# Performance work log

Hardware: AMD Instinct MI355X
Metric: run time of the kernel (lower is better)

Reference implementation:

```python
import jax, jax.numpy as jnp
import numpy as np

D_OUT = 10
N_BINS = 50
DELTA_SCALE = 60.0
TEMPERATURE = 1.0
CAND_BATCH = 1000  # hard-coded in the torch forward loop
EPS = 1e-8


def setup_inputs() -> dict:
    key = jax.random.key(0)
    ks = jax.random.split(key, 7)
    n_q, n_c, d_num, d_cat = 512, 8000, 6, 20
    return {
        "x_num": jax.random.normal(ks[0], (n_q, d_num), dtype=jnp.float32),
        "x_cat": jax.random.uniform(ks[1], (n_q, d_cat), dtype=jnp.float32),
        "candidate_x_num": jax.random.normal(ks[2], (n_c, d_num), dtype=jnp.float32),
        "candidate_x_cat": jax.random.uniform(ks[3], (n_c, d_cat), dtype=jnp.float32),
        "candidate_y": jax.random.randint(ks[4], (n_c,), 0, D_OUT, dtype=jnp.int64),
        # delta = rand(d_in_num, n_bins) * delta_scale (Parameter init)
        "delta": jax.random.uniform(ks[5], (d_num, N_BINS), dtype=jnp.float32) * DELTA_SCALE,
        # u = rand(d_in_num, n_bins) (buffer)
        "u": jax.random.uniform(ks[6], (d_num, N_BINS), dtype=jnp.float32),
    }


def _feature_map(x, delta, u):
    # x: [N, d_num] -> bin indices [N, d_num * n_bins]
    scaled_u = u * delta  # [d_num, n_bins]
    bins = jnp.ceil((x[:, :, None] - scaled_u[None]) / delta[None])
    return bins.reshape(x.shape[0], -1)


def reference(x_num, x_cat, candidate_x_num, candidate_x_cat, candidate_y, delta, u):
    x_enc = jnp.concatenate([_feature_map(x_num, delta, u), x_cat], axis=1)          # [Nq, D]
    c_enc = jnp.concatenate([_feature_map(candidate_x_num, delta, u), candidate_x_cat], axis=1)  # [Nc, D]
    y_oh = jax.nn.one_hot(candidate_y, D_OUT, dtype=jnp.float32)                     # [Nc, d_out]

    n_c, d = c_enc.shape
    n_chunks = n_c // CAND_BATCH
    c_chunks = c_enc.reshape(n_chunks, CAND_BATCH, d)
    y_chunks = y_oh.reshape(n_chunks, CAND_BATCH, D_OUT)

    def step(carry, batch):
        logits, lse = carry
        cx, cy = batch
        # L1 cdist: [Nq, CAND_BATCH]
        dist = jnp.sum(jnp.abs(x_enc[:, None, :] - cx[None, :, :]), axis=-1) / TEMPERATURE
        logits = logits + jnp.exp(-dist) @ cy
        # NOTE: faithful to torch code — per-batch logsumexp values are SUMMED
        lse = lse + jax.nn.logsumexp(-dist, axis=1)
        return (logits, lse), None

    n_q = x_enc.shape[0]
    init = (jnp.zeros((n_q, D_OUT), jnp.float32), jnp.zeros((n_q,), jnp.float32))
    (logits, lse), _ = jax.lax.scan(step, init, (c_chunks, y_chunks))
    return jnp.log(logits + EPS) - lse[:, None]
```

## Files before the change

kernel.cpp:

```cpp
#include <hip/hip_runtime.h>
#include <math.h>

#define NQ 512
#define NC 8000
#define DNUM 6
#define NBINS 50
#define DCAT 20
#define DENC 26
#define DOUT 10
#define CHUNK 1000
#define NCHUNK 8
#define QT 8
#define PSTRIDE 12

__global__ void encode(const float* __restrict__ c_num, const float* __restrict__ c_cat,
                       const float* __restrict__ x_num, const float* __restrict__ x_cat,
                       const float* __restrict__ delta, const float* __restrict__ u,
                       float* __restrict__ cEnc, float* __restrict__ qEnc) {
    int i = blockIdx.x * 256 + threadIdx.x;
    const int nA = (NC + NQ) * DNUM;
    const int nB = (NC + NQ) * DCAT;
    if (i < nA) {
        int f = i % DNUM, p = i / DNUM;
        bool is_c = p < NC;
        int idx = is_c ? p : p - NC;
        float v = (is_c ? c_num : x_num)[idx * DNUM + f];
        float g = 0.f;
        for (int j = 0; j < NBINS; ++j) {
            float dl = delta[f * NBINS + j];
            float sc = u[f * NBINS + j] * dl;
            g += ceilf((v - sc) / dl);
        }
        if (is_c) cEnc[f * NC + idx] = g;
        else      qEnc[f * NQ + idx] = g;
    } else if (i < nA + nB) {
        int i2 = i - nA;
        int k = i2 % DCAT, p = i2 / DCAT;
        bool is_c = p < NC;
        int idx = is_c ? p : p - NC;
        float v = (is_c ? c_cat : x_cat)[idx * DCAT + k];
        if (is_c) cEnc[(DNUM + k) * NC + idx] = v;
        else      qEnc[(DNUM + k) * NQ + idx] = v;
    }
}

__global__ __launch_bounds__(256) void dist_k(
    const float* __restrict__ cEnc, const float* __restrict__ qEnc,
    float* __restrict__ D) {
    __shared__ float xs[DENC * QT];
    const int tid = threadIdx.x;
    const int c = blockIdx.x * 256 + tid;
    const int q0 = blockIdx.y * QT;

    if (tid < DENC * QT) {
        int d = tid >> 3, q = tid & 7;
        xs[tid] = qEnc[d * NQ + q0 + q];
    }
    __syncthreads();

    const int cc = (c < NC) ? c : NC - 1;
    float cv[DENC];
#pragma unroll
    for (int d = 0; d < DENC; ++d) cv[d] = cEnc[(size_t)d * NC + cc];

    float acc[QT];
#pragma unroll
    for (int q = 0; q < QT; ++q) acc[q] = 0.f;
#pragma unroll
    for (int d = 0; d < DENC; ++d) {
        float cvd = cv[d];
        const float* xv = xs + d * QT;
#pragma unroll
        for (int q = 0; q < QT; ++q) acc[q] += fabsf(cvd - xv[q]);
    }
    if (c < NC) {
#pragma unroll
        for (int q = 0; q < QT; ++q) D[(size_t)(q0 + q) * NC + c] = acc[q];
    }
}

__global__ __launch_bounds__(256) void reduce_k(
    const float* __restrict__ D, const int* __restrict__ cy,
    float* __restrict__ parts) {
    __shared__ float wr[4][12];
    __shared__ float m_sh;

    const int tid = threadIdx.x;
    const int chunk = blockIdx.x;
    const int q = blockIdx.y;
    const int lane = tid & 63, wave = tid >> 6;

    const bool act = (tid < CHUNK / 4);
    const int base = chunk * CHUNK + (act ? 4 * tid : CHUNK - 4);
    float4 dv = *(const float4*)(D + (size_t)q * NC + base);
    int4 yv = *(const int4*)(cy + base);

    float v = act ? fminf(fminf(dv.x, dv.y), fminf(dv.z, dv.w)) : INFINITY;
#pragma unroll
    for (int m = 32; m >= 1; m >>= 1) v = fminf(v, __shfl_xor(v, m));
    if (lane == 0) wr[wave][0] = v;
    __syncthreads();
    if (tid == 0)
        m_sh = fminf(fminf(wr[0][0], wr[1][0]), fminf(wr[2][0], wr[3][0]));
    __syncthreads();
    const float m = m_sh;

    float r[11];
#pragma unroll
    for (int k = 0; k < 11; ++k) r[k] = 0.f;
    if (act) {
        float e0 = __expf(-dv.x), e1 = __expf(-dv.y),
              e2 = __expf(-dv.z), e3 = __expf(-dv.w);
#pragma unroll
        for (int k = 0; k < DOUT; ++k) {
            r[k] = (yv.x == k ? e0 : 0.f) + (yv.y == k ? e1 : 0.f) +
                   (yv.z == k ? e2 : 0.f) + (yv.w == k ? e3 : 0.f);
        }
        r[10] = __expf(m - dv.x) + __expf(m - dv.y) +
                __expf(m - dv.z) + __expf(m - dv.w);
    }
#pragma unroll
    for (int k = 0; k < 11; ++k) {
        float s = r[k];
#pragma unroll
        for (int mm = 32; mm >= 1; mm >>= 1) s += __shfl_xor(s, mm);
        if (lane == 0) wr[wave][k] = s;
    }
    __syncthreads();
    if (tid < 11) {
        float s = wr[0][tid] + wr[1][tid] + wr[2][tid] + wr[3][tid];
        parts[((size_t)q * NCHUNK + chunk) * PSTRIDE + tid] = s;
    }
    if (tid == 11)
        parts[((size_t)q * NCHUNK + chunk) * PSTRIDE + 11] = m;
}

__global__ void finalize(const float* __restrict__ parts, float* __restrict__ out) {
    int q = blockIdx.x * 256 + threadIdx.x;
    if (q >= NQ) return;
    float logits[DOUT];
#pragma unroll
    for (int k = 0; k < DOUT; ++k) logits[k] = 0.f;
    float lse = 0.f;
#pragma unroll
    for (int ch = 0; ch < NCHUNK; ++ch) {
        const float* p = parts + ((size_t)q * NCHUNK + ch) * PSTRIDE;
#pragma unroll
        for (int k = 0; k < DOUT; ++k) logits[k] += p[k];
        lse += logf(p[10]) - p[11];
    }
#pragma unroll
    for (int k = 0; k < DOUT; ++k)
        out[q * DOUT + k] = logf(logits[k] + 1e-8f) - lse;
}

extern "C" void kernel_launch(void* const* d_in, const int* in_sizes, int n_in,
                              void* d_out, int out_size, void* d_ws, size_t ws_size,
                              hipStream_t stream) {
    const float* x_num = (const float*)d_in[0];
    const float* x_cat = (const float*)d_in[1];
    const float* c_num = (const float*)d_in[2];
    const float* c_cat = (const float*)d_in[3];
    const int*   c_y   = (const int*)d_in[4];
    const float* delta = (const float*)d_in[5];
    const float* u     = (const float*)d_in[6];

    float* ws = (float*)d_ws;
    float* cEnc = ws;
    float* qEnc = cEnc + (size_t)DENC * NC;
    float* Dmat = qEnc + (size_t)DENC * NQ;
    float* parts = Dmat + (size_t)NQ * NC;

    const int total = (NC + NQ) * DENC;
    encode<<<(total + 255) / 256, 256, 0, stream>>>(
        c_num, c_cat, x_num, x_cat, delta, u, cEnc, qEnc);
    dist_k<<<dim3((NC + 255) / 256, NQ / QT), 256, 0, stream>>>(cEnc, qEnc, Dmat);
    reduce_k<<<dim3(NCHUNK, NQ), 256, 0, stream>>>(Dmat, c_y, parts);
    finalize<<<(NQ + 255) / 256, 256, 0, stream>>>(parts, (float*)d_out);
}
```

Before: 104.9 us.

## Fuse distance, chunk reduction and finalize into one per-query-pair kernel

Replaces the three-kernel pipeline (distance matrix written to global memory, per-chunk reduction, finalize) with a single kernel where each block handles two queries across all chunks. Distances are computed in registers and immediately reduced, so the 16 MB distance matrix round-trip and two launches go away. The in-chunk max is now combined from per-wave minima with rescaling. The trade-off is that each block rereads the whole candidate encoding with only two queries of reuse, and the launch has fewer, larger blocks.

New measurement: 105.9 us. About the same (+1.0%).

```diff
diff --git a/kernel.cpp b/kernel.cpp
--- a/kernel.cpp
+++ b/kernel.cpp
@@ -10,8 +10,6 @@
 #define DOUT 10
 #define CHUNK 1000
 #define NCHUNK 8
-#define QT 8
-#define PSTRIDE 12
 
 __global__ void encode(const float* __restrict__ c_num, const float* __restrict__ c_cat,
                        const float* __restrict__ x_num, const float* __restrict__ x_cat,
@@ -44,114 +42,111 @@
     }
 }
 
-__global__ __launch_bounds__(256) void dist_k(
+__global__ __launch_bounds__(512) void nca_all(
     const float* __restrict__ cEnc, const float* __restrict__ qEnc,
-    float* __restrict__ D) {
-    __shared__ float xs[DENC * QT];
+    const int* __restrict__ cy, float* __restrict__ out) {
+    __shared__ float xs[DENC * 2];
+    __shared__ float parts[NCHUNK * 8 * 24];
+    __shared__ float tmp[2][NCHUNK];
+    __shared__ float lse_sh[2];
+
     const int tid = threadIdx.x;
-    const int c = blockIdx.x * 256 + tid;
-    const int q0 = blockIdx.y * QT;
-
-    if (tid < DENC * QT) {
-        int d = tid >> 3, q = tid & 7;
+    const int q0 = blockIdx.x * 2;
+    if (tid < DENC * 2) {
+        int d = tid >> 1, q = tid & 1;
         xs[tid] = qEnc[d * NQ + q0 + q];
     }
     __syncthreads();
 
-    const int cc = (c < NC) ? c : NC - 1;
-    float cv[DENC];
-#pragma unroll
-    for (int d = 0; d < DENC; ++d) cv[d] = cEnc[(size_t)d * NC + cc];
-
-    float acc[QT];
-#pragma unroll
-    for (int q = 0; q < QT; ++q) acc[q] = 0.f;
-#pragma unroll
-    for (int d = 0; d < DENC; ++d) {
-        float cvd = cv[d];
-        const float* xv = xs + d * QT;
-#pragma unroll
-        for (int q = 0; q < QT; ++q) acc[q] += fabsf(cvd - xv[q]);
-    }
-    if (c < NC) {
-#pragma unroll
-        for (int q = 0; q < QT; ++q) D[(size_t)(q0 + q) * NC + c] = acc[q];
-    }
-}
-
-__global__ __launch_bounds__(256) void reduce_k(
-    const float* __restrict__ D, const int* __restrict__ cy,
-    float* __restrict__ parts) {
-    __shared__ float wr[4][12];
-    __shared__ float m_sh;
-
-    const int tid = threadIdx.x;
-    const int chunk = blockIdx.x;
-    const int q = blockIdx.y;
+    const bool act = tid < 500;
+    const int cl = act ? 2 * tid : 996;
     const int lane = tid & 63, wave = tid >> 6;
 
-    const bool act = (tid < CHUNK / 4);
-    const int base = chunk * CHUNK + (act ? 4 * tid : CHUNK - 4);
-    float4 dv = *(const float4*)(D + (size_t)q * NC + base);
-    int4 yv = *(const int4*)(cy + base);
+    for (int chunk = 0; chunk < NCHUNK; ++chunk) {
+        const float* cp = cEnc + chunk * CHUNK + cl;
+        float2 cv[DENC];
+#pragma unroll
+        for (int d = 0; d < DENC; ++d) cv[d] = *(const float2*)(cp + (size_t)d * NC);
 
-    float v = act ? fminf(fminf(dv.x, dv.y), fminf(dv.z, dv.w)) : INFINITY;
+        float a00 = 0.f, a01 = 0.f, a10 = 0.f, a11 = 0.f;
 #pragma unroll
-    for (int m = 32; m >= 1; m >>= 1) v = fminf(v, __shfl_xor(v, m));
-    if (lane == 0) wr[wave][0] = v;
-    __syncthreads();
-    if (tid == 0)
-        m_sh = fminf(fminf(wr[0][0], wr[1][0]), fminf(wr[2][0], wr[3][0]));
-    __syncthreads();
-    const float m = m_sh;
+        for (int d = 0; d < DENC; ++d) {
+            float x0 = xs[2 * d], x1 = xs[2 * d + 1];
+            a00 += fabsf(cv[d].x - x0); a01 += fabsf(cv[d].y - x0);
+            a10 += fabsf(cv[d].x - x1); a11 += fabsf(cv[d].y - x1);
+        }
 
-    float r[11];
+        float m0 = act ? fminf(a00, a01) : INFINITY;
+        float m1 = act ? fminf(a10, a11) : INFINITY;
 #pragma unroll
-    for (int k = 0; k < 11; ++k) r[k] = 0.f;
-    if (act) {
-        float e0 = __expf(-dv.x), e1 = __expf(-dv.y),
-              e2 = __expf(-dv.z), e3 = __expf(-dv.w);
+        for (int sh = 32; sh >= 1; sh >>= 1) {
+            m0 = fminf(m0, __shfl_xor(m0, sh));
+            m1 = fminf(m1, __shfl_xor(m1, sh));
+        }
+
+        int2 y = *(const int2*)(cy + chunk * CHUNK + cl);
+        float e00 = 0.f, e01 = 0.f, e10 = 0.f, e11 = 0.f, s0 = 0.f, s1 = 0.f;
+        if (act) {
+            e00 = __expf(-a00); e01 = __expf(-a01);
+            e10 = __expf(-a10); e11 = __expf(-a11);
+            s0 = __expf(m0 - a00) + __expf(m0 - a01);
+            s1 = __expf(m1 - a10) + __expf(m1 - a11);
+        }
+
+        float r[22];
 #pragma unroll
         for (int k = 0; k < DOUT; ++k) {
-            r[k] = (yv.x == k ? e0 : 0.f) + (yv.y == k ? e1 : 0.f) +
-                   (yv.z == k ? e2 : 0.f) + (yv.w == k ? e3 : 0.f);
+            r[k]      = (y.x == k ? e00 : 0.f) + (y.y == k ? e01 : 0.f);
+            r[11 + k] = (y.x == k ? e10 : 0.f) + (y.y == k ? e11 : 0.f);
         }
-        r[10] = __expf(m - dv.x) + __expf(m - dv.y) +
-                __expf(m - dv.z) + __expf(m - dv.w);
-    }
+        r[10] = s0; r[21] = s1;
 #pragma unroll
-    for (int k = 0; k < 11; ++k) {
-        float s = r[k];
+        for (int k = 0; k < 22; ++k) {
 #pragma unroll
-        for (int mm = 32; mm >= 1; mm >>= 1) s += __shfl_xor(s, mm);
-        if (lane == 0) wr[wave][k] = s;
+            for (int sh = 32; sh >= 1; sh >>= 1) r[k] += __shfl_xor(r[k], sh);
+        }
+        if (lane == 0) {
+            float* p = parts + chunk * 192 + wave * 24;
+            p[0] = m0; p[1] = r[10];
+#pragma unroll
+            for (int k = 0; k < DOUT; ++k) p[2 + k] = r[k];
+            p[12] = m1; p[13] = r[21];
+#pragma unroll
+            for (int k = 0; k < DOUT; ++k) p[14 + k] = r[11 + k];
+        }
     }
     __syncthreads();
-    if (tid < 11) {
-        float s = wr[0][tid] + wr[1][tid] + wr[2][tid] + wr[3][tid];
-        parts[((size_t)q * NCHUNK + chunk) * PSTRIDE + tid] = s;
+
+    if (tid < 16) {
+        int q = tid & 1, ch = tid >> 1;
+        const float* p = parts + ch * 192 + q * 12;
+        float M = INFINITY;
+#pragma unroll
+        for (int w = 0; w < 8; ++w) M = fminf(M, p[w * 24]);
+        float S = 0.f;
+#pragma unroll
+        for (int w = 0; w < 8; ++w) S += __expf(M - p[w * 24]) * p[w * 24 + 1];
+        tmp[q][ch] = logf(S) - M;
     }
-    if (tid == 11)
-        parts[((size_t)q * NCHUNK + chunk) * PSTRIDE + 11] = m;
-}
-
-__global__ void finalize(const float* __restrict__ parts, float* __restrict__ out) {
-    int q = blockIdx.x * 256 + threadIdx.x;
-    if (q >= NQ) return;
-    float logits[DOUT];
+    __syncthreads();
+    if (tid < 2) {
+        float l = 0.f;
 #pragma unroll
-    for (int k = 0; k < DOUT; ++k) logits[k] = 0.f;
-    float lse = 0.f;
+        for (int ch = 0; ch < NCHUNK; ++ch) l += tmp[tid][ch];
+        lse_sh[tid] = l;
+    }
+    __syncthreads();
+    if (tid < 2 * DOUT) {
+        int q = tid / DOUT, k = tid % DOUT;
+        float s = 0.f;
 #pragma unroll
-    for (int ch = 0; ch < NCHUNK; ++ch) {
-        const float* p = parts + ((size_t)q * NCHUNK + ch) * PSTRIDE;
+        for (int ch = 0; ch < NCHUNK; ++ch) {
+            const float* p = parts + ch * 192 + q * 12 + 2 + k;
 #pragma unroll
-        for (int k = 0; k < DOUT; ++k) logits[k] += p[k];
-        lse += logf(p[10]) - p[11];
+            for (int w = 0; w < 8; ++w) s += p[w * 24];
+        }
+        out[(q0 + q) * DOUT + k] = logf(s + 1e-8f) - lse_sh[q];
     }
-#pragma unroll
-    for (int k = 0; k < DOUT; ++k)
-        out[q * DOUT + k] = logf(logits[k] + 1e-8f) - lse;
 }
 
 extern "C" void kernel_launch(void* const* d_in, const int* in_sizes, int n_in,
@@ -168,13 +163,9 @@
     float* ws = (float*)d_ws;
     float* cEnc = ws;
     float* qEnc = cEnc + (size_t)DENC * NC;
-    float* Dmat = qEnc + (size_t)DENC * NQ;
-    float* parts = Dmat + (size_t)NQ * NC;
 
     const int total = (NC + NQ) * DENC;
     encode<<<(total + 255) / 256, 256, 0, stream>>>(
         c_num, c_cat, x_num, x_cat, delta, u, cEnc, qEnc);
-    dist_k<<<dim3((NC + 255) / 256, NQ / QT), 256, 0, stream>>>(cEnc, qEnc, Dmat);
-    reduce_k<<<dim3(NCHUNK, NQ), 256, 0, stream>>>(Dmat, c_y, parts);
-    finalize<<<(NQ + 255) / 256, 256, 0, stream>>>(parts, (float*)d_out);
+    nca_all<<<NQ / 2, 512, 0, stream>>>(cEnc, qEnc, c_y, (float*)d_out);
 }
```
